# Optimization experiments

Measured on AMD Instinct MI355X. Metric: run time of the kernel, lower is better.

Reference implementation:

```python
import jax, jax.numpy as jnp
import numpy as np

NUM_EXPERTS = 8
TOP_K = 2
HIDDEN = 1024
NUM_TOKENS = 8192


def setup_inputs() -> dict:
    key = jax.random.key(0)
    k1, k2, k3 = jax.random.split(key, 3)
    x = jax.random.normal(k1, (NUM_TOKENS, HIDDEN), dtype=jnp.float32)
    # gate: nn.Linear(hidden, num_experts, bias=False) -> weight [E, H]
    gate_w = jax.random.normal(k2, (NUM_EXPERTS, HIDDEN), dtype=jnp.float32) * 0.02
    # experts: nn.Linear(hidden, hidden, bias=False) stacked -> [E, H_out, H_in]
    expert_w = jax.random.normal(k3, (NUM_EXPERTS, HIDDEN, HIDDEN), dtype=jnp.float32) * 0.02
    return {"x": x, "gate_w": gate_w, "expert_w": expert_w}


def reference(x, gate_w, expert_w):
    # --- routing ---
    logits = jnp.einsum("th,eh->te", x, gate_w)          # [T, E]
    probs = jax.nn.softmax(logits, axis=-1)
    weights, indices = jax.lax.top_k(probs, TOP_K)        # [T, K], [T, K]

    # --- expert compute (equivalent of dispatch + per-expert GEMM) ---
    # y_e = x @ W_e^T for every expert; tokens then gather their top-k rows.
    all_y = jnp.einsum("td,ehd->eth", x, expert_w)        # [E, T, H]

    # --- weighted combine (gather by routed expert ids) ---
    t_idx = jnp.arange(x.shape[0])[None, :]               # [1, T]
    y_sel = all_y[indices.T, t_idx, :]                    # [K, T, H]
    out = jnp.einsum("tk,kth->th", weights, y_sel)        # [T, H]
    return out
```

## Files before the change

kernel.cpp:

```cpp
#include <hip/hip_runtime.h>
#include <hip/hip_bf16.h>
#include <stdint.h>

#define NUM_TOKENS 8192
#define HIDDEN 1024
#define NEXP 8
#define TOPK 2

typedef __bf16 bf16;
typedef __bf16 bf16x4 __attribute__((ext_vector_type(4)));
typedef __bf16 bf16x8 __attribute__((ext_vector_type(8)));
typedef float f32x4 __attribute__((ext_vector_type(4)));

__device__ __forceinline__ void gld_lds16(const void* g, void* l) {
  __builtin_amdgcn_global_load_lds(
      (const __attribute__((address_space(1))) void*)(uintptr_t)g,
      (__attribute__((address_space(3))) void*)(uint32_t)(uintptr_t)l,
      16, 0, 0);
}

__global__ __launch_bounds__(256) void gate_route_kernel(
    const float* __restrict__ x, const float* __restrict__ gw,
    bf16* __restrict__ xbf, int* __restrict__ echoice, float* __restrict__ pchoice)
{
  const int wid  = threadIdx.x >> 6;
  const int lane = threadIdx.x & 63;
  const int t = blockIdx.x * 4 + wid;

  const float* xrow = x + (size_t)t * HIDDEN;
  bf16* xbrow = xbf + (size_t)t * HIDDEN;

  float acc[NEXP];
#pragma unroll
  for (int e = 0; e < NEXP; ++e) acc[e] = 0.f;

#pragma unroll
  for (int it = 0; it < 4; ++it) {
    const int idx = it * 256 + lane * 4;
    float4 xv = *(const float4*)(xrow + idx);
    bf16x4 xb;
    xb[0] = (bf16)xv.x; xb[1] = (bf16)xv.y; xb[2] = (bf16)xv.z; xb[3] = (bf16)xv.w;
    *(bf16x4*)(xbrow + idx) = xb;
#pragma unroll
    for (int e = 0; e < NEXP; ++e) {
      float4 gv = *(const float4*)(gw + e * HIDDEN + idx);
      acc[e] += xv.x * gv.x + xv.y * gv.y + xv.z * gv.z + xv.w * gv.w;
    }
  }
#pragma unroll
  for (int e = 0; e < NEXP; ++e) {
#pragma unroll
    for (int off = 32; off > 0; off >>= 1)
      acc[e] += __shfl_xor(acc[e], off, 64);
  }

  if (lane == 0) {
    float m = acc[0];
#pragma unroll
    for (int e = 1; e < NEXP; ++e) m = fmaxf(m, acc[e]);
    float p[NEXP]; float s = 0.f;
#pragma unroll
    for (int e = 0; e < NEXP; ++e) { p[e] = expf(acc[e] - m); s += p[e]; }
    const float inv = 1.f / s;
#pragma unroll
    for (int e = 0; e < NEXP; ++e) p[e] *= inv;
    int i0 = 0; float p0 = p[0];
#pragma unroll
    for (int e = 1; e < NEXP; ++e) if (p[e] > p0) { p0 = p[e]; i0 = e; }
    int i1 = -1; float p1 = -1.f;
#pragma unroll
    for (int e = 0; e < NEXP; ++e) if (e != i0 && p[e] > p1) { p1 = p[e]; i1 = e; }

    echoice[t]              = i0;
    echoice[NUM_TOKENS + t] = i1;
    pchoice[t]              = p0;
    pchoice[NUM_TOKENS + t] = p1;
  }
}

__global__ __launch_bounds__(1024) void build_lists_kernel(
    const int* __restrict__ echoice, const float* __restrict__ pchoice,
    int* __restrict__ cnt, int* __restrict__ tok, float* __restrict__ wt)
{
  const int list = blockIdx.x;
  const int k = list >> 3;
  const int e = list & 7;
  const int tid  = threadIdx.x;
  const int wave = tid >> 6;
  const int lane = tid & 63;
  const int tbase = wave * 512;

  const int*   ec = echoice + k * NUM_TOKENS;
  const float* pc = pchoice + k * NUM_TOKENS;

  __shared__ int wcnt[16];
  __shared__ int woff[16];

  const unsigned long long lower = ((unsigned long long)1 << lane) - 1;

  int   ev[8];
  float pv[8];
#pragma unroll
  for (int c = 0; c < 8; ++c) {
    ev[c] = ec[tbase + c * 64 + lane];
    pv[c] = pc[tbase + c * 64 + lane];
  }
  unsigned long long m[8];
  int cl = 0;
#pragma unroll
  for (int c = 0; c < 8; ++c) { m[c] = __ballot(ev[c] == e); cl += __popcll(m[c]); }
  if (lane == 0) wcnt[wave] = cl;
  __syncthreads();
  if (tid == 0) {
    int off = 0;
#pragma unroll
    for (int w = 0; w < 16; ++w) { woff[w] = off; off += wcnt[w]; }
    cnt[list] = off;
  }
  __syncthreads();
  int run = woff[wave];
#pragma unroll
  for (int c = 0; c < 8; ++c) {
    if (ev[c] == e) {
      const int pos = run + __popcll(m[c] & lower);
      tok[(size_t)list * NUM_TOKENS + pos] = tbase + c * 64 + lane;
      wt [(size_t)list * NUM_TOKENS + pos] = pv[c];
    }
    run += __popcll(m[c]);
  }
}

__global__ __launch_bounds__(256) void convert_w_kernel(
    const float* __restrict__ w, bf16* __restrict__ wbf)
{
  const size_t i = ((size_t)blockIdx.x * 256 + threadIdx.x) * 4;
  float4 v = *(const float4*)(w + i);
  bf16x4 b;
  b[0] = (bf16)v.x; b[1] = (bf16)v.y; b[2] = (bf16)v.z; b[3] = (bf16)v.w;
  *(bf16x4*)(wbf + i) = b;
}

__global__ __launch_bounds__(256) void moe_gemm_kernel(
    const bf16* __restrict__ xbf, const bf16* __restrict__ wbf,
    const int* __restrict__ cnt, const int* __restrict__ tok,
    const float* __restrict__ wt, float* __restrict__ out)
{
  const int e  = blockIdx.z >> 1;
  const int k  = blockIdx.z & 1;
  const int list = k * NEXP + e;
  const int mt = blockIdx.y;
  const int nt = blockIdx.x;
  const int count = cnt[list];
  const int m0 = mt * 128;
  if (m0 >= count) return;
  const int rows = min(128, count - m0);

  __shared__ __align__(16) bf16 As[2 * 128 * 64];
  __shared__ __align__(16) bf16 Bs[2 * 128 * 64];
  __shared__ int   tok_s[128];
  __shared__ float wt_s[128];

  const int tid = threadIdx.x;
  if (tid < 128) {
    if (tid < rows) {
      tok_s[tid] = tok[(size_t)list * NUM_TOKENS + m0 + tid];
      wt_s[tid]  = wt [(size_t)list * NUM_TOKENS + m0 + tid];
    } else { tok_s[tid] = 0; wt_s[tid] = 0.f; }
  }
  __syncthreads();

  const int csrc = (tid & 7) ^ ((tid >> 3) & 7);
  const bf16* aptr[4];
  const bf16* bptr[4];
  const size_t eoff = (size_t)e * HIDDEN * HIDDEN;
#pragma unroll
  for (int p = 0; p < 4; ++p) {
    const int r = p * 32 + (tid >> 3);
    aptr[p] = xbf + (size_t)tok_s[r] * HIDDEN + csrc * 8;
    bptr[p] = wbf + eoff + (size_t)(nt * 128 + r) * HIDDEN + csrc * 8;
  }
  bf16* la = As + tid * 8;
  bf16* lb = Bs + tid * 8;

  const int wid  = tid >> 6;
  const int lane = tid & 63;
  const int wm = (wid >> 1) * 64;
  const int wn = (wid & 1) * 64;
  const int qm = lane & 15;
  const int l4 = lane >> 4;

  f32x4 acc[4][4];
#pragma unroll
  for (int i = 0; i < 4; ++i)
#pragma unroll
    for (int j = 0; j < 4; ++j) acc[i][j] = (f32x4){0.f, 0.f, 0.f, 0.f};

#pragma unroll
  for (int p = 0; p < 4; ++p) {
    gld_lds16(aptr[p], la + p * 2048);
    gld_lds16(bptr[p], lb + p * 2048);
  }
  __syncthreads();

  for (int t = 0; t < 16; ++t) {
    const int cur = t & 1;
    if (t < 15) {
      const int kc = (t + 1) * 64;
      bf16* lan = la + (cur ^ 1) * 8192;
      bf16* lbn = lb + (cur ^ 1) * 8192;
#pragma unroll
      for (int p = 0; p < 4; ++p) {
        gld_lds16(aptr[p] + kc, lan + p * 2048);
        gld_lds16(bptr[p] + kc, lbn + p * 2048);
      }
    }

    const bf16* Ab = As + cur * 8192;
    const bf16* Bb = Bs + cur * 8192;
    bf16x8 a[4][2], b[4][2];
#pragma unroll
    for (int i = 0; i < 4; ++i) {
      const int r = wm + i * 16 + qm;
      const int x7 = r & 7;
      a[i][0] = *(const bf16x8*)(Ab + r * 64 + (l4 ^ x7) * 8);
      a[i][1] = *(const bf16x8*)(Ab + r * 64 + ((4 + l4) ^ x7) * 8);
    }
#pragma unroll
    for (int j = 0; j < 4; ++j) {
      const int r = wn + j * 16 + qm;
      const int x7 = r & 7;
      b[j][0] = *(const bf16x8*)(Bb + r * 64 + (l4 ^ x7) * 8);
      b[j][1] = *(const bf16x8*)(Bb + r * 64 + ((4 + l4) ^ x7) * 8);
    }
#pragma unroll
    for (int h = 0; h < 2; ++h)
#pragma unroll
      for (int i = 0; i < 4; ++i)
#pragma unroll
        for (int j = 0; j < 4; ++j)
          acc[i][j] = __builtin_amdgcn_mfma_f32_16x16x32_bf16(a[i][h], b[j][h], acc[i][j], 0, 0, 0);

    if (t < 15) __syncthreads();
  }

  const int h0 = nt * 128 + wn + (lane & 15);
#pragma unroll
  for (int i = 0; i < 4; ++i) {
    const int rbase = wm + i * 16 + (lane >> 4) * 4;
#pragma unroll
    for (int r = 0; r < 4; ++r) {
      const int rl = rbase + r;
      if (rl < rows) {
        const int t = tok_s[rl];
        const float w = wt_s[rl];
        float* orow = out + (size_t)t * HIDDEN + h0;
#pragma unroll
        for (int j = 0; j < 4; ++j) {
          const float v = w * acc[i][j][r];
          unsafeAtomicAdd(orow + j * 16, v);
        }
      }
    }
  }
}

extern "C" void kernel_launch(void* const* d_in, const int* in_sizes, int n_in,
                              void* d_out, int out_size, void* d_ws, size_t ws_size,
                              hipStream_t stream) {
  const float* x  = (const float*)d_in[0];
  const float* gw = (const float*)d_in[1];
  const float* ew = (const float*)d_in[2];
  float* out = (float*)d_out;

  char* ws = (char*)d_ws;
  int*   cnt     = (int*)ws;
  int*   echoice = (int*)(ws + 256);
  float* pchoice = (float*)(ws + 256 + (size_t)2 * NUM_TOKENS * 4);
  int*   tok = (int*)(ws + 256 + (size_t)4 * NUM_TOKENS * 4);
  float* wt  = (float*)(ws + 256 + (size_t)20 * NUM_TOKENS * 4);
  bf16*  xbf = (bf16*)(ws + 256 + (size_t)36 * NUM_TOKENS * 4);
  bf16*  wbf = (bf16*)((char*)xbf + (size_t)NUM_TOKENS * HIDDEN * 2);

  hipMemsetAsync(out, 0, (size_t)NUM_TOKENS * HIDDEN * sizeof(float), stream);

  gate_route_kernel<<<NUM_TOKENS / 4, 256, 0, stream>>>(x, gw, xbf, echoice, pchoice);
  build_lists_kernel<<<2 * NEXP, 1024, 0, stream>>>(echoice, pchoice, cnt, tok, wt);
  convert_w_kernel<<<(NEXP * HIDDEN * HIDDEN) / (4 * 256), 256, 0, stream>>>(ew, wbf);

  dim3 grid(HIDDEN / 128, NUM_TOKENS / 128, 2 * NEXP);
  moe_gemm_kernel<<<grid, 256, 0, stream>>>(xbf, wbf, cnt, tok, wt, out);
}
```

Before: 210.1 us.

## Fuse prep kernels and deepen GEMM pipeline to four stages of K=32

Merges gating/routing, the expert-weight bf16 conversion and the zeroing of the output into one prep kernel, so three launches and a memset become one. The MoE GEMM moves from a double-buffered K=64 tile to a four-stage ring of K=32 tiles, with explicit vmcnt waits, raw barriers and s_setprio around the MFMA block. The goal is to hide global-to-LDS load latency and cut launch overhead, at the cost of more barriers per K and hand-tuned waitcnt counts that must match the issued loads exactly.

```diff
diff --git a/kernel.cpp b/kernel.cpp
--- a/kernel.cpp
+++ b/kernel.cpp
@@ -19,62 +19,90 @@
       16, 0, 0);
 }
 
-__global__ __launch_bounds__(256) void gate_route_kernel(
+__global__ __launch_bounds__(256) void prep_kernel(
     const float* __restrict__ x, const float* __restrict__ gw,
-    bf16* __restrict__ xbf, int* __restrict__ echoice, float* __restrict__ pchoice)
+    const float* __restrict__ ew,
+    bf16* __restrict__ xbf, bf16* __restrict__ wbf,
+    int* __restrict__ echoice, float* __restrict__ pchoice,
+    float* __restrict__ out)
 {
-  const int wid  = threadIdx.x >> 6;
-  const int lane = threadIdx.x & 63;
-  const int t = blockIdx.x * 4 + wid;
-
-  const float* xrow = x + (size_t)t * HIDDEN;
-  bf16* xbrow = xbf + (size_t)t * HIDDEN;
-
-  float acc[NEXP];
-#pragma unroll
-  for (int e = 0; e < NEXP; ++e) acc[e] = 0.f;
-
-#pragma unroll
-  for (int it = 0; it < 4; ++it) {
-    const int idx = it * 256 + lane * 4;
-    float4 xv = *(const float4*)(xrow + idx);
-    bf16x4 xb;
-    xb[0] = (bf16)xv.x; xb[1] = (bf16)xv.y; xb[2] = (bf16)xv.z; xb[3] = (bf16)xv.w;
-    *(bf16x4*)(xbrow + idx) = xb;
+  const int b   = blockIdx.x;
+  const int tid = threadIdx.x;
+
+  if (b < 2048) {
+    const int wid  = tid >> 6;
+    const int lane = tid & 63;
+    const int t = b * 4 + wid;
+
+    const float* xrow = x + (size_t)t * HIDDEN;
+    bf16* xbrow = xbf + (size_t)t * HIDDEN;
+
+    float acc[NEXP];
+#pragma unroll
+    for (int e = 0; e < NEXP; ++e) acc[e] = 0.f;
+
+#pragma unroll
+    for (int it = 0; it < 4; ++it) {
+      const int idx = it * 256 + lane * 4;
+      float4 xv = *(const float4*)(xrow + idx);
+      bf16x4 xb;
+      xb[0] = (bf16)xv.x; xb[1] = (bf16)xv.y; xb[2] = (bf16)xv.z; xb[3] = (bf16)xv.w;
+      *(bf16x4*)(xbrow + idx) = xb;
+#pragma unroll
+      for (int e = 0; e < NEXP; ++e) {
+        float4 gv = *(const float4*)(gw + e * HIDDEN + idx);
+        acc[e] += xv.x * gv.x + xv.y * gv.y + xv.z * gv.z + xv.w * gv.w;
+      }
+    }
 #pragma unroll
     for (int e = 0; e < NEXP; ++e) {
-      float4 gv = *(const float4*)(gw + e * HIDDEN + idx);
-      acc[e] += xv.x * gv.x + xv.y * gv.y + xv.z * gv.z + xv.w * gv.w;
-    }
-  }
-#pragma unroll
-  for (int e = 0; e < NEXP; ++e) {
-#pragma unroll
-    for (int off = 32; off > 0; off >>= 1)
-      acc[e] += __shfl_xor(acc[e], off, 64);
-  }
-
-  if (lane == 0) {
-    float m = acc[0];
-#pragma unroll
-    for (int e = 1; e < NEXP; ++e) m = fmaxf(m, acc[e]);
-    float p[NEXP]; float s = 0.f;
-#pragma unroll
-    for (int e = 0; e < NEXP; ++e) { p[e] = expf(acc[e] - m); s += p[e]; }
-    const float inv = 1.f / s;
-#pragma unroll
-    for (int e = 0; e < NEXP; ++e) p[e] *= inv;
-    int i0 = 0; float p0 = p[0];
-#pragma unroll
-    for (int e = 1; e < NEXP; ++e) if (p[e] > p0) { p0 = p[e]; i0 = e; }
-    int i1 = -1; float p1 = -1.f;
-#pragma unroll
-    for (int e = 0; e < NEXP; ++e) if (e != i0 && p[e] > p1) { p1 = p[e]; i1 = e; }
-
-    echoice[t]              = i0;
-    echoice[NUM_TOKENS + t] = i1;
-    pchoice[t]              = p0;
-    pchoice[NUM_TOKENS + t] = p1;
+#pragma unroll
+      for (int off = 32; off > 0; off >>= 1)
+        acc[e] += __shfl_xor(acc[e], off, 64);
+    }
+
+    if (lane == 0) {
+      float m = acc[0];
+#pragma unroll
+      for (int e = 1; e < NEXP; ++e) m = fmaxf(m, acc[e]);
+      float p[NEXP]; float s = 0.f;
+#pragma unroll
+      for (int e = 0; e < NEXP; ++e) { p[e] = expf(acc[e] - m); s += p[e]; }
+      const float inv = 1.f / s;
+#pragma unroll
+      for (int e = 0; e < NEXP; ++e) p[e] *= inv;
+      int i0 = 0; float p0 = p[0];
+#pragma unroll
+      for (int e = 1; e < NEXP; ++e) if (p[e] > p0) { p0 = p[e]; i0 = e; }
+      int i1 = -1; float p1 = -1.f;
+#pragma unroll
+      for (int e = 0; e < NEXP; ++e) if (e != i0 && p[e] > p1) { p1 = p[e]; i1 = e; }
+
+      echoice[t]              = i0;
+      echoice[NUM_TOKENS + t] = i1;
+      pchoice[t]              = p0;
+      pchoice[NUM_TOKENS + t] = p1;
+    }
+  } else if (b < 4096) {
+    const size_t i = ((size_t)(b - 2048) * 256 + tid) * 16;
+    float4 v0 = *(const float4*)(ew + i);
+    float4 v1 = *(const float4*)(ew + i + 4);
+    float4 v2 = *(const float4*)(ew + i + 8);
+    float4 v3 = *(const float4*)(ew + i + 12);
+    bf16x8 o0, o1;
+    o0[0] = (bf16)v0.x; o0[1] = (bf16)v0.y; o0[2] = (bf16)v0.z; o0[3] = (bf16)v0.w;
+    o0[4] = (bf16)v1.x; o0[5] = (bf16)v1.y; o0[6] = (bf16)v1.z; o0[7] = (bf16)v1.w;
+    o1[0] = (bf16)v2.x; o1[1] = (bf16)v2.y; o1[2] = (bf16)v2.z; o1[3] = (bf16)v2.w;
+    o1[4] = (bf16)v3.x; o1[5] = (bf16)v3.y; o1[6] = (bf16)v3.z; o1[7] = (bf16)v3.w;
+    *(bf16x8*)(wbf + i)     = o0;
+    *(bf16x8*)(wbf + i + 8) = o1;
+  } else {
+    const size_t i = ((size_t)(b - 4096) * 256 + tid) * 16;
+    const float4 z = {0.f, 0.f, 0.f, 0.f};
+    *(float4*)(out + i)      = z;
+    *(float4*)(out + i + 4)  = z;
+    *(float4*)(out + i + 8)  = z;
+    *(float4*)(out + i + 12) = z;
   }
 }
 
@@ -128,16 +156,6 @@
     }
     run += __popcll(m[c]);
   }
-}
-
-__global__ __launch_bounds__(256) void convert_w_kernel(
-    const float* __restrict__ w, bf16* __restrict__ wbf)
-{
-  const size_t i = ((size_t)blockIdx.x * 256 + threadIdx.x) * 4;
-  float4 v = *(const float4*)(w + i);
-  bf16x4 b;
-  b[0] = (bf16)v.x; b[1] = (bf16)v.y; b[2] = (bf16)v.z; b[3] = (bf16)v.w;
-  *(bf16x4*)(wbf + i) = b;
 }
 
 __global__ __launch_bounds__(256) void moe_gemm_kernel(
@@ -155,8 +173,8 @@
   if (m0 >= count) return;
   const int rows = min(128, count - m0);
 
-  __shared__ __align__(16) bf16 As[2 * 128 * 64];
-  __shared__ __align__(16) bf16 Bs[2 * 128 * 64];
+  __shared__ __align__(16) bf16 As[4][128 * 32];
+  __shared__ __align__(16) bf16 Bs[4][128 * 32];
   __shared__ int   tok_s[128];
   __shared__ float wt_s[128];
 
@@ -169,18 +187,23 @@
   }
   __syncthreads();
 
-  const int csrc = (tid & 7) ^ ((tid >> 3) & 7);
-  const bf16* aptr[4];
-  const bf16* bptr[4];
-  const size_t eoff = (size_t)e * HIDDEN * HIDDEN;
-#pragma unroll
-  for (int p = 0; p < 4; ++p) {
-    const int r = p * 32 + (tid >> 3);
-    aptr[p] = xbf + (size_t)tok_s[r] * HIDDEN + csrc * 8;
-    bptr[p] = wbf + eoff + (size_t)(nt * 128 + r) * HIDDEN + csrc * 8;
-  }
-  bf16* la = As + tid * 8;
-  bf16* lb = Bs + tid * 8;
+  const int csrc = (((tid & 3) ^ ((tid >> 3) & 3)) << 3);
+  const int r0 = tid >> 2;
+  const bf16* gA0 = xbf + (size_t)tok_s[r0] * HIDDEN + csrc;
+  const bf16* gA1 = xbf + (size_t)tok_s[r0 + 64] * HIDDEN + csrc;
+  const bf16* gB0 = wbf + (size_t)e * HIDDEN * HIDDEN
+                  + (size_t)(nt * 128 + r0) * HIDDEN + csrc;
+  const bf16* gB1 = gB0 + (size_t)64 * HIDDEN;
+
+  auto STAGE = [&](int t, int buf) {
+    const int kc = t << 5;
+    bf16* la = &As[buf][0] + tid * 8;
+    bf16* lb = &Bs[buf][0] + tid * 8;
+    gld_lds16(gA0 + kc, la);
+    gld_lds16(gA1 + kc, la + 2048);
+    gld_lds16(gB0 + kc, lb);
+    gld_lds16(gB1 + kc, lb + 2048);
+  };
 
   const int wid  = tid >> 6;
   const int lane = tid & 63;
@@ -195,53 +218,47 @@
 #pragma unroll
     for (int j = 0; j < 4; ++j) acc[i][j] = (f32x4){0.f, 0.f, 0.f, 0.f};
 
-#pragma unroll
-  for (int p = 0; p < 4; ++p) {
-    gld_lds16(aptr[p], la + p * 2048);
-    gld_lds16(bptr[p], lb + p * 2048);
-  }
-  __syncthreads();
-
-  for (int t = 0; t < 16; ++t) {
-    const int cur = t & 1;
-    if (t < 15) {
-      const int kc = (t + 1) * 64;
-      bf16* lan = la + (cur ^ 1) * 8192;
-      bf16* lbn = lb + (cur ^ 1) * 8192;
-#pragma unroll
-      for (int p = 0; p < 4; ++p) {
-        gld_lds16(aptr[p] + kc, lan + p * 2048);
-        gld_lds16(bptr[p] + kc, lbn + p * 2048);
-      }
-    }
-
-    const bf16* Ab = As + cur * 8192;
-    const bf16* Bb = Bs + cur * 8192;
-    bf16x8 a[4][2], b[4][2];
+  auto COMPUTE = [&](int buf) {
+    const bf16* Ab = &As[buf][0];
+    const bf16* Bb = &Bs[buf][0];
+    bf16x8 a[4], b[4];
 #pragma unroll
     for (int i = 0; i < 4; ++i) {
       const int r = wm + i * 16 + qm;
-      const int x7 = r & 7;
-      a[i][0] = *(const bf16x8*)(Ab + r * 64 + (l4 ^ x7) * 8);
-      a[i][1] = *(const bf16x8*)(Ab + r * 64 + ((4 + l4) ^ x7) * 8);
+      a[i] = *(const bf16x8*)(Ab + r * 32 + ((l4 ^ ((r >> 1) & 3)) << 3));
     }
 #pragma unroll
     for (int j = 0; j < 4; ++j) {
       const int r = wn + j * 16 + qm;
-      const int x7 = r & 7;
-      b[j][0] = *(const bf16x8*)(Bb + r * 64 + (l4 ^ x7) * 8);
-      b[j][1] = *(const bf16x8*)(Bb + r * 64 + ((4 + l4) ^ x7) * 8);
-    }
-#pragma unroll
-    for (int h = 0; h < 2; ++h)
-#pragma unroll
-      for (int i = 0; i < 4; ++i)
-#pragma unroll
-        for (int j = 0; j < 4; ++j)
-          acc[i][j] = __builtin_amdgcn_mfma_f32_16x16x32_bf16(a[i][h], b[j][h], acc[i][j], 0, 0, 0);
-
-    if (t < 15) __syncthreads();
-  }
+      b[j] = *(const bf16x8*)(Bb + r * 32 + ((l4 ^ ((r >> 1) & 3)) << 3));
+    }
+    __builtin_amdgcn_s_setprio(1);
+#pragma unroll
+    for (int i = 0; i < 4; ++i)
+#pragma unroll
+      for (int j = 0; j < 4; ++j)
+        acc[i][j] = __builtin_amdgcn_mfma_f32_16x16x32_bf16(a[i], b[j], acc[i][j], 0, 0, 0);
+    __builtin_amdgcn_s_setprio(0);
+  };
+
+  STAGE(0, 0); STAGE(1, 1); STAGE(2, 2);
+
+#pragma unroll 1
+  for (int t = 0; t < 29; ++t) {
+    asm volatile("s_waitcnt vmcnt(8)" ::: "memory");
+    __builtin_amdgcn_s_barrier();
+    STAGE(t + 3, (t + 3) & 3);
+    COMPUTE(t & 3);
+  }
+  asm volatile("s_waitcnt vmcnt(8)" ::: "memory");
+  __builtin_amdgcn_s_barrier();
+  COMPUTE(1);
+  asm volatile("s_waitcnt vmcnt(4)" ::: "memory");
+  __builtin_amdgcn_s_barrier();
+  COMPUTE(2);
+  asm volatile("s_waitcnt vmcnt(0)" ::: "memory");
+  __builtin_amdgcn_s_barrier();
+  COMPUTE(3);
 
   const int h0 = nt * 128 + wn + (lane & 15);
 #pragma unroll
@@ -281,11 +298,8 @@
   bf16*  xbf = (bf16*)(ws + 256 + (size_t)36 * NUM_TOKENS * 4);
   bf16*  wbf = (bf16*)((char*)xbf + (size_t)NUM_TOKENS * HIDDEN * 2);
 
-  hipMemsetAsync(out, 0, (size_t)NUM_TOKENS * HIDDEN * sizeof(float), stream);
-
-  gate_route_kernel<<<NUM_TOKENS / 4, 256, 0, stream>>>(x, gw, xbf, echoice, pchoice);
+  prep_kernel<<<6144, 256, 0, stream>>>(x, gw, ew, xbf, wbf, echoice, pchoice, out);
   build_lists_kernel<<<2 * NEXP, 1024, 0, stream>>>(echoice, pchoice, cnt, tok, wt);
-  convert_w_kernel<<<(NEXP * HIDDEN * HIDDEN) / (4 * 256), 256, 0, stream>>>(ew, wbf);
 
   dim3 grid(HIDDEN / 128, NUM_TOKENS / 128, 2 * NEXP);
   moe_gemm_kernel<<<grid, 256, 0, stream>>>(xbf, wbf, cnt, tok, wt, out);
```

After: 204.7 us. 2.6% less time.
